# Optimization experiments

Hardware: AMD Instinct MI355X
Metric: run time of the kernel (lower is better)

Reference implementation:

```python
import jax, jax.numpy as jnp
import numpy as np

T, B, OBS, H, A = 512, 256, 128, 256, 32

def setup_inputs() -> dict:
    key = jax.random.key(0)
    ks = jax.random.split(key, 16)
    s = 0.05
    return {
        'hidden': jnp.zeros((B, H), jnp.float32),
        'obs': jax.random.normal(ks[0], (T, B, OBS), jnp.float32),
        'dones': jax.random.bernoulli(ks[1], 0.1, (T, B)),
        'avail_actions': (jax.random.uniform(ks[2], (T, B, A)) > 0.1).astype(jnp.float32),
        'W_emb': jax.random.normal(ks[3], (OBS, H), jnp.float32) * s,
        'b_emb': jnp.zeros((H,), jnp.float32),
        'Wi': jax.random.normal(ks[4], (H, 3 * H), jnp.float32) * s,
        'bi': jnp.zeros((3 * H,), jnp.float32),
        'Whr': jax.random.normal(ks[5], (H, H), jnp.float32) * s,
        'Whz': jax.random.normal(ks[6], (H, H), jnp.float32) * s,
        'Whn': jax.random.normal(ks[7], (H, H), jnp.float32) * s,
        'bhn': jnp.zeros((H,), jnp.float32),
        'W_a1': jax.random.normal(ks[8], (H, H), jnp.float32) * s,
        'b_a1': jnp.zeros((H,), jnp.float32),
        'W_a2': jax.random.normal(ks[9], (H, A), jnp.float32) * s,
        'b_a2': jnp.zeros((A,), jnp.float32),
        'W_c1': jax.random.normal(ks[10], (H, H), jnp.float32) * s,
        'b_c1': jnp.zeros((H,), jnp.float32),
        'W_c2': jax.random.normal(ks[11], (H, 1), jnp.float32) * s,
        'b_c2': jnp.zeros((1,), jnp.float32),
    }

def reference(hidden, obs, dones, avail_actions, W_emb, b_emb, Wi, bi,
              Whr, Whz, Whn, bhn, W_a1, b_a1, W_a2, b_a2, W_c1, b_c1, W_c2, b_c2):
    # obs embedding + relu: [T,B,OBS] -> [T,B,H]
    emb = jax.nn.relu(obs @ W_emb + b_emb)
    # precompute input gate projections for all timesteps (same math as per-step Dense)
    gi = emb @ Wi + bi  # [T,B,3H]

    def step(h, xs):
        gi_t, done_t = xs
        h = jnp.where(done_t[:, None], 0.0, h)  # reset-select to zero init carry
        ir, iz, inn = jnp.split(gi_t, 3, axis=-1)
        r = jax.nn.sigmoid(ir + h @ Whr)
        z = jax.nn.sigmoid(iz + h @ Whz)
        n = jnp.tanh(inn + r * (h @ Whn + bhn))
        h_new = (1.0 - z) * n + z * h
        return h_new, h_new

    hidden_out, y = jax.lax.scan(step, hidden, (gi, dones))  # y: [T,B,H]

    actor_h = jax.nn.relu(y @ W_a1 + b_a1)
    actor_mean = actor_h @ W_a2 + b_a2  # [T,B,A]
    logits = actor_mean - (1.0 - avail_actions) * 1e10

    critic_h = jax.nn.relu(y @ W_c1 + b_c1)
    value = jnp.squeeze(critic_h @ W_c2 + b_c2, axis=-1)  # [T,B]
    return hidden_out, logits, value
```

## Files before the change

### kernel.cpp

```cpp
#include <hip/hip_runtime.h>
#include <stdint.h>

#define T_DIM 512
#define B_DIM 256
#define OBS_DIM 128
#define H_DIM 256
#define A_DIM 32
#define TB (T_DIM*B_DIM)

typedef unsigned short u16;
typedef unsigned int   u32;
typedef _Float16 half2v __attribute__((ext_vector_type(2)));
typedef __attribute__((ext_vector_type(8))) short short8;
typedef __attribute__((ext_vector_type(4))) float f32x4;
typedef __attribute__((ext_vector_type(4))) u32   u32x4;

__device__ __forceinline__ float bf2f(u16 v){ return __uint_as_float(((u32)v)<<16); }
__device__ __forceinline__ u16 f2bf(float f){
    u32 x = __float_as_uint(f);
    u32 r = x + 0x7fffu + ((x>>16)&1u);
    return (u16)(r>>16);
}
__device__ __forceinline__ float2 bfpair(u32 u){
    return make_float2(__uint_as_float(u<<16), __uint_as_float(u & 0xffff0000u));
}

__device__ __forceinline__ float dot2(u32 a, u32 b, float c){
#if __has_builtin(__builtin_amdgcn_fdot2)
    return __builtin_amdgcn_fdot2(__builtin_bit_cast(half2v,a),
                                  __builtin_bit_cast(half2v,b), c, false);
#else
    half2v ha = __builtin_bit_cast(half2v,a), hb = __builtin_bit_cast(half2v,b);
    return fmaf((float)ha[0],(float)hb[0], fmaf((float)ha[1],(float)hb[1], c));
#endif
}

__global__ void zero_flags_kernel(int* p){ if(threadIdx.x<4) p[threadIdx.x]=0; }

__global__ void detect_kernel(const unsigned char* __restrict__ d, int n, int* __restrict__ flags){
    int f=0;
    for(int p = blockIdx.x*blockDim.x+threadIdx.x; p<n; p += gridDim.x*blockDim.x){
        if(d[p]){ int m=p&3; if(m==1) f|=1; else if(m>=2) f|=2; }
    }
    if(f) atomicOr(flags, f);
}

__global__ void cvt_wt_kernel(const float* __restrict__ Whr, const float* __restrict__ Whz,
                              const float* __restrict__ Whn, u32* __restrict__ dst){
    int i = blockIdx.x*blockDim.x + threadIdx.x;
    if(i >= 3*32*256*4) return;
    int e = i & 3;
    int j = (i >> 2) & 255;
    int q = (i >> 10) & 31;
    int m = i >> 15;
    const float* W = (m==0) ? Whr : (m==1) ? Whz : Whn;
    int kp = q*4 + e, k = 2*kp;
    _Float16 lo = (_Float16)W[(size_t)k    *H_DIM + j];
    _Float16 hi = (_Float16)W[(size_t)(k+1)*H_DIM + j];
    dst[i] = (u32)__builtin_bit_cast(u16,lo) | ((u32)__builtin_bit_cast(u16,hi) << 16);
}

__global__ void cvt_wT_kernel(const float* __restrict__ W, u16* __restrict__ dst,
                              int K, int N){
    int i = blockIdx.x*blockDim.x + threadIdx.x;
    if(i >= K*N) return;
    int n = i / K;
    int k = i - n*K;
    dst[i] = f2bf(W[(size_t)k*N + n]);
}

template<int RELU, int AF32>
__global__ __launch_bounds__(256, 2)
void gemm_mfma_kernel(const void* __restrict__ A_, const u16* __restrict__ Bt,
                      const float* __restrict__ bias, u16* __restrict__ C,
                      int M, int N, int K)
{
    __shared__ u16 As[128*32];
    __shared__ u16 Bs[128*32];
    const int tid  = threadIdx.x;
    const int wave = tid >> 6;
    const int lane = tid & 63;
    const int ln15 = lane & 15;
    const int quad = lane >> 4;
    const int wm = wave & 1, wn = wave >> 1;
    const int rowBase = blockIdx.y*128;
    const int colBase = blockIdx.x*128;

    f32x4 acc[4][4] = {};

    const int sr = tid >> 1;
    const int sc = (tid & 1) * 16;

    for(int kb = 0; kb < K; kb += 32){
        if(AF32){
            const float* af = (const float*)A_;
            const float* ag = af + (size_t)(rowBase+sr)*K + kb + sc;
            float4 f0 = *(const float4*)ag;
            float4 f1 = *(const float4*)(ag+4);
            float4 f2 = *(const float4*)(ag+8);
            float4 f3 = *(const float4*)(ag+12);
            u16 tmp[16] = { f2bf(f0.x),f2bf(f0.y),f2bf(f0.z),f2bf(f0.w),
                            f2bf(f1.x),f2bf(f1.y),f2bf(f1.z),f2bf(f1.w),
                            f2bf(f2.x),f2bf(f2.y),f2bf(f2.z),f2bf(f2.w),
                            f2bf(f3.x),f2bf(f3.y),f2bf(f3.z),f2bf(f3.w) };
            *(uint4*)&As[sr*32 + sc]     = *(const uint4*)&tmp[0];
            *(uint4*)&As[sr*32 + sc + 8] = *(const uint4*)&tmp[8];
        } else {
            const u16* ab = (const u16*)A_;
            const u16* ag = ab + (size_t)(rowBase+sr)*K + kb + sc;
            uint4 av0 = *(const uint4*)ag;
            uint4 av1 = *(const uint4*)(ag+8);
            *(uint4*)&As[sr*32 + sc]     = av0;
            *(uint4*)&As[sr*32 + sc + 8] = av1;
        }
        {
            const u16* bg = Bt + (size_t)(colBase+sr)*K + kb + sc;
            uint4 bv0 = *(const uint4*)bg;
            uint4 bv1 = *(const uint4*)(bg+8);
            *(uint4*)&Bs[sr*32 + sc]     = bv0;
            *(uint4*)&Bs[sr*32 + sc + 8] = bv1;
        }
        __syncthreads();

        short8 af[4], bf[4];
        #pragma unroll
        for(int mt=0;mt<4;mt++)
            af[mt] = *(const short8*)&As[(wm*64+mt*16+ln15)*32 + quad*8];
        #pragma unroll
        for(int nt=0;nt<4;nt++)
            bf[nt] = *(const short8*)&Bs[(wn*64+nt*16+ln15)*32 + quad*8];
        #pragma unroll
        for(int mt=0;mt<4;mt++){
            #pragma unroll
            for(int nt=0;nt<4;nt++){
                acc[mt][nt] = __builtin_amdgcn_mfma_f32_16x16x32_bf16(
                                  af[mt], bf[nt], acc[mt][nt], 0, 0, 0);
            }
        }
        __syncthreads();
    }

    #pragma unroll
    for(int nt=0;nt<4;nt++){
        int n = colBase + wn*64 + nt*16 + ln15;
        float bv = bias[n];
        #pragma unroll
        for(int mt=0;mt<4;mt++){
            #pragma unroll
            for(int r=0;r<4;r++){
                int m = rowBase + wm*64 + mt*16 + quad*4 + r;
                float v = acc[mt][nt][r] + bv;
                if(RELU) v = fmaxf(v, 0.f);
                C[(size_t)m*N + n] = f2bf(v);
            }
        }
    }
}

__global__ __attribute__((amdgpu_flat_work_group_size(1024,1024), amdgpu_waves_per_eu(4,4)))
void scan_kernel(const u16* __restrict__ gi, const void* __restrict__ dones,
                 const int* __restrict__ flags, const u32x4* __restrict__ Wt4,
                 const float* __restrict__ bhn, float* __restrict__ h_carry,
                 u16* __restrict__ y, int t0, int Tc)
{
    __shared__ __align__(16) u32 hbuf[2][128];
    __shared__ float rex[3][4][256];
    const int tid = threadIdx.x;
    const int j   = tid & 255;
    const int g   = tid >> 8;
    const int row = blockIdx.x;
    const int fl  = flags[0];
    const int mode = (fl&1) ? 0 : ((fl&2) ? 2 : 1);

    auto getdone = [&](int t)->bool{
        int idx = t*B_DIM + row;
        if(mode==0) return ((const unsigned char*)dones)[idx] != 0;
        if(mode==1) return ((const int*)dones)[idx] != 0;
        return ((const float*)dones)[idx] != 0.f;
    };

    const u32x4* baseR = Wt4 + (size_t)( 0 + g*8)*256 + j;
    const u32x4* baseZ = Wt4 + (size_t)(32 + g*8)*256 + j;
    const u32x4* baseN = Wt4 + (size_t)(64 + g*8)*256 + j;
    u32 wr[32], wz[32], wn[32];
    #pragma unroll
    for(int q=0;q<8;q++){
        u32x4 tr = baseR[(size_t)q*256]; wr[4*q]=tr[0]; wr[4*q+1]=tr[1]; wr[4*q+2]=tr[2]; wr[4*q+3]=tr[3];
        u32x4 tz = baseZ[(size_t)q*256]; wz[4*q]=tz[0]; wz[4*q+1]=tz[1]; wz[4*q+2]=tz[2]; wz[4*q+3]=tz[3];
        u32x4 tn = baseN[(size_t)q*256]; wn[4*q]=tn[0]; wn[4*q+1]=tn[1]; wn[4*q+2]=tn[2]; wn[4*q+3]=tn[3];
    }
    #pragma unroll
    for(int q=0;q<32;q+=4){
        asm volatile("" : "+v"(wr[q  ]),"+v"(wr[q+1]),"+v"(wr[q+2]),"+v"(wr[q+3]),
                          "+v"(wz[q  ]),"+v"(wz[q+1]),"+v"(wz[q+2]),"+v"(wz[q+3]),
                          "+v"(wn[q  ]),"+v"(wn[q+1]),"+v"(wn[q+2]),"+v"(wn[q+3]));
    }

    float bh = 0.f;
    float hoj = 0.f;
    if(g == 0){
        bh = bhn[j];
        bool d0 = getdone(t0);
        hoj = d0 ? 0.f : h_carry[(size_t)row*H_DIM + j];
        ((_Float16*)hbuf[0])[j] = (_Float16)hoj;
    }
    __syncthreads();

    int cur = 0;
    for(int t=0; t<Tc; ++t){
        size_t gbase = ((size_t)t*B_DIM + row)*768;
        float ir=0.f, izv=0.f, inn=0.f; bool dn=false;
        if(g == 0){
            ir  = bf2f(gi[gbase + j]);
            izv = bf2f(gi[gbase + 256 + j]);
            inn = bf2f(gi[gbase + 512 + j]);
            dn  = (t < Tc-1) ? getdone(t0+t+1) : false;
        }

        float r0=0.f,r1=0.f,z0=0.f,z1=0.f,n0=0.f,n1=0.f;
        const u32x4* hb = (const u32x4*)hbuf[cur] + g*8;
        #pragma unroll
        for(int q=0;q<8;q++){
            u32x4 hv = hb[q];
            r0 = dot2(wr[4*q  ], hv[0], r0); r1 = dot2(wr[4*q+1], hv[1], r1);
            r0 = dot2(wr[4*q+2], hv[2], r0); r1 = dot2(wr[4*q+3], hv[3], r1);
            z0 = dot2(wz[4*q  ], hv[0], z0); z1 = dot2(wz[4*q+1], hv[1], z1);
            z0 = dot2(wz[4*q+2], hv[2], z0); z1 = dot2(wz[4*q+3], hv[3], z1);
            n0 = dot2(wn[4*q  ], hv[0], n0); n1 = dot2(wn[4*q+1], hv[1], n1);
            n0 = dot2(wn[4*q+2], hv[2], n0); n1 = dot2(wn[4*q+3], hv[3], n1);
        }
        rex[0][g][j] = r0 + r1;
        rex[1][g][j] = z0 + z1;
        rex[2][g][j] = n0 + n1;
        __syncthreads();

        if(g == 0){
            float rt = (rex[0][0][j] + rex[0][1][j]) + (rex[0][2][j] + rex[0][3][j]);
            float zt = (rex[1][0][j] + rex[1][1][j]) + (rex[1][2][j] + rex[1][3][j]);
            float nt = (rex[2][0][j] + rex[2][1][j]) + (rex[2][2][j] + rex[2][3][j]);
            float r = 1.f/(1.f + __expf(-(ir + rt)));
            float z = 1.f/(1.f + __expf(-(izv + zt)));
            float x = inn + r*(nt + bh);
            float e2 = __expf(2.f*x);
            float n = 1.f - 2.f/(e2 + 1.f);
            float hn = (1.f - z)*n + z*hoj;
            y[((size_t)t*B_DIM + row)*H_DIM + j] = f2bf(hn);
            hoj = dn ? 0.f : hn;
            ((_Float16*)hbuf[cur^1])[j] = (_Float16)hoj;
        }
        __syncthreads();
        cur ^= 1;
    }

    if(g == 0) h_carry[(size_t)row*H_DIM + j] = hoj;
}

__global__ __launch_bounds__(256)
void actor2_kernel(const u16* __restrict__ ah, const float* __restrict__ W_a2,
                   const float* __restrict__ b_a2, const float* __restrict__ avail,
                   float* __restrict__ logits)
{
    __shared__ u16 ahs[64][264];
    const int tid = threadIdx.x;
    const int r0 = blockIdx.x*64;
    {
        int row = tid & 63;
        int c0 = (tid >> 6) * 64;
        const uint4* gp = (const uint4*)(ah + (size_t)(r0+row)*H_DIM + c0);
        #pragma unroll
        for(int q=0;q<8;q++){
            uint4 u = gp[q];
            u32* dst = (u32*)&ahs[row][c0 + q*8];
            dst[0]=u.x; dst[1]=u.y; dst[2]=u.z; dst[3]=u.w;
        }
    }
    __syncthreads();
    const int c  = tid & 31;
    const int rg = tid >> 5;
    float acc[8]={0.f,0.f,0.f,0.f,0.f,0.f,0.f,0.f};
    float bc = b_a2[c];
    for(int k=0;k<H_DIM;k+=4){
        float w0 = W_a2[(k+0)*A_DIM + c];
        float w1 = W_a2[(k+1)*A_DIM + c];
        float w2 = W_a2[(k+2)*A_DIM + c];
        float w3 = W_a2[(k+3)*A_DIM + c];
        #pragma unroll
        for(int rr=0;rr<8;rr++){
            uint2 av = *(const uint2*)&ahs[rg*8+rr][k];
            float2 p0 = bfpair(av.x), p1 = bfpair(av.y);
            acc[rr] = fmaf(p0.x,w0,fmaf(p0.y,w1,fmaf(p1.x,w2,fmaf(p1.y,w3,acc[rr]))));
        }
    }
    #pragma unroll
    for(int rr=0;rr<8;rr++){
        int grow = r0 + rg*8 + rr;
        float av = avail[(size_t)grow*A_DIM + c];
        logits[(size_t)grow*A_DIM + c] = acc[rr] + bc - (1.f-av)*1e10f;
    }
}

__global__ __launch_bounds__(256)
void critic2_kernel(const u16* __restrict__ ch, const float* __restrict__ W_c2,
                    const float* __restrict__ b_c2, float* __restrict__ value)
{
    const int lane = threadIdx.x & 63;
    const int wid  = threadIdx.x >> 6;
    const int row  = blockIdx.x*4 + wid;
    uint2 av = *(const uint2*)(ch + (size_t)row*H_DIM + lane*4);
    float2 p0 = bfpair(av.x), p1 = bfpair(av.y);
    float4 wv = *(const float4*)(W_c2 + lane*4);
    float acc = p0.x*wv.x + p0.y*wv.y + p1.x*wv.z + p1.y*wv.w;
    #pragma unroll
    for(int off=32; off>0; off>>=1) acc += __shfl_down(acc, off, 64);
    if(lane==0) value[row] = acc + b_c2[0];
}

extern "C" void kernel_launch(void* const* d_in, const int* in_sizes, int n_in,
                              void* d_out, int out_size, void* d_ws, size_t ws_size,
                              hipStream_t stream)
{
    const float* hidden = (const float*)d_in[0];
    const float* obs    = (const float*)d_in[1];
    const void*  dones  = d_in[2];
    const float* avail  = (const float*)d_in[3];
    const float* W_emb  = (const float*)d_in[4];
    const float* b_emb  = (const float*)d_in[5];
    const float* Wi     = (const float*)d_in[6];
    const float* bi     = (const float*)d_in[7];
    const float* Whr    = (const float*)d_in[8];
    const float* Whz    = (const float*)d_in[9];
    const float* Whn    = (const float*)d_in[10];
    const float* bhn    = (const float*)d_in[11];
    const float* W_a1   = (const float*)d_in[12];
    const float* b_a1   = (const float*)d_in[13];
    const float* W_a2   = (const float*)d_in[14];
    const float* b_a2   = (const float*)d_in[15];
    const float* W_c1   = (const float*)d_in[16];
    const float* b_c1   = (const float*)d_in[17];
    const float* W_c2   = (const float*)d_in[18];
    const float* b_c2   = (const float*)d_in[19];

    float* out_hidden = (float*)d_out;
    float* out_logits = out_hidden + (size_t)B_DIM*H_DIM;
    float* out_value  = out_logits + (size_t)TB*A_DIM;

    const size_t fixed = 393216 + 393216 + 131072 + 131072 + 65536 + 262144 + 256;
    int Tc = 4;
    for(int cand = 64; cand >= 4; cand >>= 1){
        size_t need = fixed + (size_t)cand*(393216  + 2*131072 );
        if(need <= ws_size){ Tc = cand; break; }
    }
    const int NC = T_DIM / Tc;

    uint8_t* ws = (uint8_t*)d_ws;
    size_t off = 0;
    u32*  wt_b    = (u32*)(ws + off); off += 393216;
    u16*  wiT     = (u16*)(ws + off); off += 393216;
    u16*  wa1T    = (u16*)(ws + off); off += 131072;
    u16*  wc1T    = (u16*)(ws + off); off += 131072;
    u16*  wembT   = (u16*)(ws + off); off += 65536;
    float* h_carry= (float*)(ws + off); off += 262144;
    int*  flags   = (int*)(ws + off); off += 256;
    u16*  gi_c    = (u16*)(ws + off); off += (size_t)Tc*393216;
    u16*  emb_c   = (u16*)(ws + off); off += (size_t)Tc*131072;
    u16*  y_c     = (u16*)(ws + off); off += (size_t)Tc*131072;
    u16*  ah_c    = emb_c;
    u16*  ch_c    = emb_c;

    zero_flags_kernel<<<1, 64, 0, stream>>>(flags);
    detect_kernel<<<64, 256, 0, stream>>>((const unsigned char*)dones, TB, flags);
    cvt_wt_kernel<<<384, 256, 0, stream>>>(Whr, Whz, Whn, wt_b);
    cvt_wT_kernel<<<768, 256, 0, stream>>>(Wi,   wiT,  256, 768);
    cvt_wT_kernel<<<256, 256, 0, stream>>>(W_a1, wa1T, 256, 256);
    cvt_wT_kernel<<<256, 256, 0, stream>>>(W_c1, wc1T, 256, 256);
    cvt_wT_kernel<<<128, 256, 0, stream>>>(W_emb, wembT, 128, 256);
    hipMemcpyAsync(h_carry, hidden, (size_t)B_DIM*H_DIM*sizeof(float),
                   hipMemcpyDeviceToDevice, stream);

    const int Mc = Tc*B_DIM;
    const int gy = Mc/128;

    for(int c = 0; c < NC; ++c){
        const int t0 = c*Tc;
        const float* obs_c = obs + (size_t)t0*B_DIM*OBS_DIM;
        gemm_mfma_kernel<1,1><<<dim3(2,gy), 256, 0, stream>>>(obs_c, wembT, b_emb, emb_c, Mc, 256, 128);
        gemm_mfma_kernel<0,0><<<dim3(6,gy), 256, 0, stream>>>(emb_c, wiT, bi, gi_c, Mc, 768, 256);
        scan_kernel<<<256, 1024, 0, stream>>>(gi_c, dones, flags, (const u32x4*)wt_b,
                                              bhn, h_carry, y_c, t0, Tc);
        gemm_mfma_kernel<1,0><<<dim3(2,gy), 256, 0, stream>>>(y_c, wa1T, b_a1, ah_c, Mc, 256, 256);
        actor2_kernel<<<Mc/64, 256, 0, stream>>>(ah_c, W_a2, b_a2,
                                                 avail + (size_t)t0*B_DIM*A_DIM,
                                                 out_logits + (size_t)t0*B_DIM*A_DIM);
        gemm_mfma_kernel<1,0><<<dim3(2,gy), 256, 0, stream>>>(y_c, wc1T, b_c1, ch_c, Mc, 256, 256);
        critic2_kernel<<<Mc/4, 256, 0, stream>>>(ch_c, W_c2, b_c2, out_value + (size_t)t0*B_DIM);
    }

    hipMemcpyAsync(out_hidden, h_carry, (size_t)B_DIM*H_DIM*sizeof(float),
                   hipMemcpyDeviceToDevice, stream);
}
```

Before: 1.383 ms.

## Fuse actor/critic hidden GEMMs and move scan Whn weights to LDS

The actor and critic first-layer weights and biases are concatenated so that one N=512 GEMM produces both hidden activations, and the actor2/critic2 kernels read them with a row stride of 512. In the scan kernel the Whn weights are staged in shared memory (128 KB) instead of registers, which cuts VGPR pressure, at the cost of an LDS read of the weights on every step. Together these remove one GEMM launch per chunk and change the register/LDS balance of the latency-bound recurrent loop.

```diff
diff --git a/kernel.cpp b/kernel.cpp
--- a/kernel.cpp
+++ b/kernel.cpp
@@ -43,6 +43,13 @@
         if(d[p]){ int m=p&3; if(m==1) f|=1; else if(m>=2) f|=2; }
     }
     if(f) atomicOr(flags, f);
+}
+
+__global__ void concat_bias_kernel(const float* __restrict__ a, const float* __restrict__ b,
+                                   float* __restrict__ dst){
+    int i = threadIdx.x;
+    dst[i] = a[i];
+    dst[256 + i] = b[i];
 }
 
 __global__ void cvt_wt_kernel(const float* __restrict__ Whr, const float* __restrict__ Whz,
@@ -163,6 +170,7 @@
                  const float* __restrict__ bhn, float* __restrict__ h_carry,
                  u16* __restrict__ y, int t0, int Tc)
 {
+    __shared__ __align__(16) u32 nw_lds[32*256*4/4*4];
     __shared__ __align__(16) u32 hbuf[2][128];
     __shared__ float rex[3][4][256];
     const int tid = threadIdx.x;
@@ -182,18 +190,22 @@
     const u32x4* baseR = Wt4 + (size_t)( 0 + g*8)*256 + j;
     const u32x4* baseZ = Wt4 + (size_t)(32 + g*8)*256 + j;
     const u32x4* baseN = Wt4 + (size_t)(64 + g*8)*256 + j;
-    u32 wr[32], wz[32], wn[32];
+    u32 wr[32], wz[32];
     #pragma unroll
     for(int q=0;q<8;q++){
         u32x4 tr = baseR[(size_t)q*256]; wr[4*q]=tr[0]; wr[4*q+1]=tr[1]; wr[4*q+2]=tr[2]; wr[4*q+3]=tr[3];
         u32x4 tz = baseZ[(size_t)q*256]; wz[4*q]=tz[0]; wz[4*q+1]=tz[1]; wz[4*q+2]=tz[2]; wz[4*q+3]=tz[3];
-        u32x4 tn = baseN[(size_t)q*256]; wn[4*q]=tn[0]; wn[4*q+1]=tn[1]; wn[4*q+2]=tn[2]; wn[4*q+3]=tn[3];
+    }
+    {
+        u32x4* nl = (u32x4*)nw_lds;
+        #pragma unroll
+        for(int q=0;q<8;q++)
+            nl[(size_t)(g*8+q)*256 + j] = baseN[(size_t)q*256];
     }
     #pragma unroll
     for(int q=0;q<32;q+=4){
         asm volatile("" : "+v"(wr[q  ]),"+v"(wr[q+1]),"+v"(wr[q+2]),"+v"(wr[q+3]),
-                          "+v"(wz[q  ]),"+v"(wz[q+1]),"+v"(wz[q+2]),"+v"(wz[q+3]),
-                          "+v"(wn[q  ]),"+v"(wn[q+1]),"+v"(wn[q+2]),"+v"(wn[q+3]));
+                          "+v"(wz[q  ]),"+v"(wz[q+1]),"+v"(wz[q+2]),"+v"(wz[q+3]));
     }
 
     float bh = 0.f;
@@ -219,15 +231,17 @@
 
         float r0=0.f,r1=0.f,z0=0.f,z1=0.f,n0=0.f,n1=0.f;
         const u32x4* hb = (const u32x4*)hbuf[cur] + g*8;
+        const u32x4* nb = (const u32x4*)nw_lds + (size_t)(g*8)*256 + j;
         #pragma unroll
         for(int q=0;q<8;q++){
             u32x4 hv = hb[q];
+            u32x4 nv = nb[(size_t)q*256];
             r0 = dot2(wr[4*q  ], hv[0], r0); r1 = dot2(wr[4*q+1], hv[1], r1);
             r0 = dot2(wr[4*q+2], hv[2], r0); r1 = dot2(wr[4*q+3], hv[3], r1);
             z0 = dot2(wz[4*q  ], hv[0], z0); z1 = dot2(wz[4*q+1], hv[1], z1);
             z0 = dot2(wz[4*q+2], hv[2], z0); z1 = dot2(wz[4*q+3], hv[3], z1);
-            n0 = dot2(wn[4*q  ], hv[0], n0); n1 = dot2(wn[4*q+1], hv[1], n1);
-            n0 = dot2(wn[4*q+2], hv[2], n0); n1 = dot2(wn[4*q+3], hv[3], n1);
+            n0 = dot2(nv[0], hv[0], n0); n1 = dot2(nv[1], hv[1], n1);
+            n0 = dot2(nv[2], hv[2], n0); n1 = dot2(nv[3], hv[3], n1);
         }
         rex[0][g][j] = r0 + r1;
         rex[1][g][j] = z0 + z1;
@@ -256,7 +270,7 @@
 }
 
 __global__ __launch_bounds__(256)
-void actor2_kernel(const u16* __restrict__ ah, const float* __restrict__ W_a2,
+void actor2_kernel(const u16* __restrict__ ah, int ld, const float* __restrict__ W_a2,
                    const float* __restrict__ b_a2, const float* __restrict__ avail,
                    float* __restrict__ logits)
 {
@@ -266,7 +280,7 @@
     {
         int row = tid & 63;
         int c0 = (tid >> 6) * 64;
-        const uint4* gp = (const uint4*)(ah + (size_t)(r0+row)*H_DIM + c0);
+        const uint4* gp = (const uint4*)(ah + (size_t)(r0+row)*ld + c0);
         #pragma unroll
         for(int q=0;q<8;q++){
             uint4 u = gp[q];
@@ -300,13 +314,13 @@
 }
 
 __global__ __launch_bounds__(256)
-void critic2_kernel(const u16* __restrict__ ch, const float* __restrict__ W_c2,
+void critic2_kernel(const u16* __restrict__ ch, int ld, const float* __restrict__ W_c2,
                     const float* __restrict__ b_c2, float* __restrict__ value)
 {
     const int lane = threadIdx.x & 63;
     const int wid  = threadIdx.x >> 6;
     const int row  = blockIdx.x*4 + wid;
-    uint2 av = *(const uint2*)(ch + (size_t)row*H_DIM + lane*4);
+    uint2 av = *(const uint2*)(ch + (size_t)row*ld + lane*4);
     float2 p0 = bfpair(av.x), p1 = bfpair(av.y);
     float4 wv = *(const float4*)(W_c2 + lane*4);
     float acc = p0.x*wv.x + p0.y*wv.y + p1.x*wv.z + p1.y*wv.w;
@@ -344,10 +358,10 @@
     float* out_logits = out_hidden + (size_t)B_DIM*H_DIM;
     float* out_value  = out_logits + (size_t)TB*A_DIM;
 
-    const size_t fixed = 393216 + 393216 + 131072 + 131072 + 65536 + 262144 + 256;
+    const size_t fixed = 393216 + 393216 + 262144 + 65536 + 262144 + 256 + 2048;
     int Tc = 4;
     for(int cand = 64; cand >= 4; cand >>= 1){
-        size_t need = fixed + (size_t)cand*(393216  + 2*131072 );
+        size_t need = fixed + (size_t)cand*(393216  + 262144  + 131072 );
         if(need <= ws_size){ Tc = cand; break; }
     }
     const int NC = T_DIM / Tc;
@@ -356,24 +370,25 @@
     size_t off = 0;
     u32*  wt_b    = (u32*)(ws + off); off += 393216;
     u16*  wiT     = (u16*)(ws + off); off += 393216;
-    u16*  wa1T    = (u16*)(ws + off); off += 131072;
-    u16*  wc1T    = (u16*)(ws + off); off += 131072;
+    u16*  wacT    = (u16*)(ws + off); off += 262144;
     u16*  wembT   = (u16*)(ws + off); off += 65536;
     float* h_carry= (float*)(ws + off); off += 262144;
     int*  flags   = (int*)(ws + off); off += 256;
+    float* b_ac   = (float*)(ws + off); off += 2048;
     u16*  gi_c    = (u16*)(ws + off); off += (size_t)Tc*393216;
-    u16*  emb_c   = (u16*)(ws + off); off += (size_t)Tc*131072;
+    u16*  embac_c = (u16*)(ws + off); off += (size_t)Tc*262144;
     u16*  y_c     = (u16*)(ws + off); off += (size_t)Tc*131072;
-    u16*  ah_c    = emb_c;
-    u16*  ch_c    = emb_c;
+    u16*  emb_c   = embac_c;
+    u16*  ac_c    = embac_c;
 
     zero_flags_kernel<<<1, 64, 0, stream>>>(flags);
     detect_kernel<<<64, 256, 0, stream>>>((const unsigned char*)dones, TB, flags);
     cvt_wt_kernel<<<384, 256, 0, stream>>>(Whr, Whz, Whn, wt_b);
     cvt_wT_kernel<<<768, 256, 0, stream>>>(Wi,   wiT,  256, 768);
-    cvt_wT_kernel<<<256, 256, 0, stream>>>(W_a1, wa1T, 256, 256);
-    cvt_wT_kernel<<<256, 256, 0, stream>>>(W_c1, wc1T, 256, 256);
+    cvt_wT_kernel<<<256, 256, 0, stream>>>(W_a1, wacT,          256, 256);
+    cvt_wT_kernel<<<256, 256, 0, stream>>>(W_c1, wacT + 65536,  256, 256);
     cvt_wT_kernel<<<128, 256, 0, stream>>>(W_emb, wembT, 128, 256);
+    concat_bias_kernel<<<1, 256, 0, stream>>>(b_a1, b_c1, b_ac);
     hipMemcpyAsync(h_carry, hidden, (size_t)B_DIM*H_DIM*sizeof(float),
                    hipMemcpyDeviceToDevice, stream);
 
@@ -387,12 +402,12 @@
         gemm_mfma_kernel<0,0><<<dim3(6,gy), 256, 0, stream>>>(emb_c, wiT, bi, gi_c, Mc, 768, 256);
         scan_kernel<<<256, 1024, 0, stream>>>(gi_c, dones, flags, (const u32x4*)wt_b,
                                               bhn, h_carry, y_c, t0, Tc);
-        gemm_mfma_kernel<1,0><<<dim3(2,gy), 256, 0, stream>>>(y_c, wa1T, b_a1, ah_c, Mc, 256, 256);
-        actor2_kernel<<<Mc/64, 256, 0, stream>>>(ah_c, W_a2, b_a2,
+        gemm_mfma_kernel<1,0><<<dim3(4,gy), 256, 0, stream>>>(y_c, wacT, b_ac, ac_c, Mc, 512, 256);
+        actor2_kernel<<<Mc/64, 256, 0, stream>>>(ac_c, 512, W_a2, b_a2,
                                                  avail + (size_t)t0*B_DIM*A_DIM,
                                                  out_logits + (size_t)t0*B_DIM*A_DIM);
-        gemm_mfma_kernel<1,0><<<dim3(2,gy), 256, 0, stream>>>(y_c, wc1T, b_c1, ch_c, Mc, 256, 256);
-        critic2_kernel<<<Mc/4, 256, 0, stream>>>(ch_c, W_c2, b_c2, out_value + (size_t)t0*B_DIM);
+        critic2_kernel<<<Mc/4, 256, 0, stream>>>(ac_c + 256, 512, W_c2, b_c2,
+                                                 out_value + (size_t)t0*B_DIM);
     }
 
     hipMemcpyAsync(out_hidden, h_carry, (size_t)B_DIM*H_DIM*sizeof(float),
```

Result: no change. 1.360 ms (-1.7%).
